# Kernel optimization log

Hardware: AMD Instinct MI355X
Metric: run time of the kernel (lower is better)

The kernel has to match this reference:

```python
import jax, jax.numpy as jnp
import numpy as np


def _pairwise_l2(x):
    # x: [N, D] -> [N, N] Euclidean distances, matching (x_i - x_j).norm(dim=-1)
    sq = jnp.sum(x * x, axis=-1)                      # [N]
    sqd = sq[:, None] + sq[None, :] - 2.0 * (x @ x.T)  # [N, N] squared distances
    sqd = jnp.maximum(sqd, 0.0)
    # safe sqrt: zero distance (diagonal) -> 0 with zero gradient, matching
    # torch's norm subgradient at 0
    pos = sqd > 0.0
    return jnp.where(pos, jnp.sqrt(jnp.where(pos, sqd, 1.0)), 0.0)


def setup_inputs() -> dict:
    key = jax.random.key(0)
    data = jax.random.normal(key, (8192, 256), dtype=jnp.float32)
    return {"data": data}


def reference(data) -> jnp.ndarray:
    x = data.reshape(data.shape[0], -1)               # [N, D]
    dist = _pairwise_l2(x)                            # [N, N]
    denom = jax.lax.stop_gradient(jnp.sum(dist, axis=1, keepdims=True))
    return dist / denom
```

## Files before the change

kernel.cpp:

```cpp
#include <hip/hip_runtime.h>
#include <stdint.h>

#define NN 8192
#define DD 256

typedef __attribute__((ext_vector_type(8))) short short8;
typedef __attribute__((ext_vector_type(4))) float f32x4;

typedef const uint32_t __attribute__((address_space(1)))* gbl_ptr_t;
typedef uint32_t __attribute__((address_space(3)))* lds_ptr_t;

__device__ __forceinline__ void gl_lds16(const void* g, const void* l) {
    __builtin_amdgcn_global_load_lds((gbl_ptr_t)(uintptr_t)g,
                                     (lds_ptr_t)(uintptr_t)l, 16, 0, 0);
}

__device__ __forceinline__ unsigned short f32_to_bf16(float f) {
    uint32_t u = __float_as_uint(f);
    u += 0x7fff + ((u >> 16) & 1);
    return (unsigned short)(u >> 16);
}
__device__ __forceinline__ float bf16_to_f32(unsigned short h) {
    return __uint_as_float(((uint32_t)h) << 16);
}

__global__ void prep_kernel(const float* __restrict__ x,
                            unsigned short* __restrict__ hi,
                            unsigned short* __restrict__ lo,
                            float* __restrict__ sq,
                            float* __restrict__ denom) {
    const int r = blockIdx.x;
    const int t = threadIdx.x;
    float v = x[(size_t)r * DD + t];
    unsigned short h = f32_to_bf16(v);
    unsigned short l = f32_to_bf16(v - bf16_to_f32(h));
    int csw = (t & ~63) | ((((t >> 3) & 7) ^ (r & 7)) << 3) | (t & 7);
    hi[(size_t)r * DD + csw] = h;
    lo[(size_t)r * DD + csw] = l;

    float s = v * v;
    #pragma unroll
    for (int m = 32; m >= 1; m >>= 1) s += __shfl_xor(s, m, 64);
    __shared__ float ws[4];
    if ((t & 63) == 0) ws[t >> 6] = s;
    __syncthreads();
    if (t == 0) {
        sq[r] = ws[0] + ws[1] + ws[2] + ws[3];
        denom[r] = 0.0f;
    }
}

__launch_bounds__(256, 2)
__global__ void dist_kernel(const unsigned short* __restrict__ hi,
                            const unsigned short* __restrict__ lo,
                            const float* __restrict__ sq,
                            float* __restrict__ out,
                            float* __restrict__ denom) {
    __shared__ __align__(16) unsigned short lds[4 * 128 * 64];
    unsigned short* ldsAhi = lds;
    unsigned short* ldsAlo = lds + 8192;
    unsigned short* ldsBhi = lds + 16384;
    unsigned short* ldsBlo = lds + 24576;

    const int tid  = threadIdx.x;
    const int lane = tid & 63;
    const int wid  = tid >> 6;
    const int wm = wid >> 1, wn = wid & 1;
    const int l15 = lane & 15, lk = lane >> 4;

    const int row0 = blockIdx.y * 128;
    const int col0 = blockIdx.x * 128;

    f32x4 acc[4][4];
    #pragma unroll
    for (int a = 0; a < 4; ++a)
        #pragma unroll
        for (int b = 0; b < 4; ++b) acc[a][b] = (f32x4){0.f, 0.f, 0.f, 0.f};

    float rsq[4][4], csq[4];
    #pragma unroll
    for (int fm = 0; fm < 4; ++fm)
        #pragma unroll
        for (int r = 0; r < 4; ++r)
            rsq[fm][r] = sq[row0 + wm * 64 + fm * 16 + lk * 4 + r];
    #pragma unroll
    for (int fn = 0; fn < 4; ++fn)
        csq[fn] = sq[col0 + wn * 64 + fn * 16 + l15];

    for (int kt = 0; kt < 4; ++kt) {
        #pragma unroll
        for (int c = 0; c < 4; ++c) {
            int lin  = c * 256 + tid;
            int row  = lin >> 3;
            int col8 = lin & 7;
            size_t goffA = (size_t)(row0 + row) * DD + kt * 64 + col8 * 8;
            size_t goffB = (size_t)(col0 + row) * DD + kt * 64 + col8 * 8;
            size_t lbyte = (size_t)(c * 256 + wid * 64) * 16;
            gl_lds16(hi + goffA, (const char*)ldsAhi + lbyte);
            gl_lds16(lo + goffA, (const char*)ldsAlo + lbyte);
            gl_lds16(hi + goffB, (const char*)ldsBhi + lbyte);
            gl_lds16(lo + goffB, (const char*)ldsBlo + lbyte);
        }
        __syncthreads();

        #pragma unroll
        for (int ks = 0; ks < 2; ++ks) {
            short8 ah[4], al[4], bh[4], bl[4];
            #pragma unroll
            for (int fm = 0; fm < 4; ++fm) {
                int row = wm * 64 + fm * 16 + l15;
                int cb  = (ks * 64 + lk * 16) ^ ((row & 7) << 4);
                int off = row * 64 + (cb >> 1);
                ah[fm] = *(const short8*)(ldsAhi + off);
                al[fm] = *(const short8*)(ldsAlo + off);
            }
            #pragma unroll
            for (int fn = 0; fn < 4; ++fn) {
                int row = wn * 64 + fn * 16 + l15;
                int cb  = (ks * 64 + lk * 16) ^ ((row & 7) << 4);
                int off = row * 64 + (cb >> 1);
                bh[fn] = *(const short8*)(ldsBhi + off);
                bl[fn] = *(const short8*)(ldsBlo + off);
            }
            #pragma unroll
            for (int fm = 0; fm < 4; ++fm)
                #pragma unroll
                for (int fn = 0; fn < 4; ++fn) {
                    acc[fm][fn] = __builtin_amdgcn_mfma_f32_16x16x32_bf16(
                        ah[fm], bh[fn], acc[fm][fn], 0, 0, 0);
                    acc[fm][fn] = __builtin_amdgcn_mfma_f32_16x16x32_bf16(
                        ah[fm], bl[fn], acc[fm][fn], 0, 0, 0);
                    acc[fm][fn] = __builtin_amdgcn_mfma_f32_16x16x32_bf16(
                        al[fm], bh[fn], acc[fm][fn], 0, 0, 0);
                }
        }
        __syncthreads();
    }

    float rp[4][4];
    #pragma unroll
    for (int a = 0; a < 4; ++a)
        #pragma unroll
        for (int b = 0; b < 4; ++b) rp[a][b] = 0.f;

    #pragma unroll
    for (int fm = 0; fm < 4; ++fm) {
        #pragma unroll
        for (int fn = 0; fn < 4; ++fn) {
            #pragma unroll
            for (int r = 0; r < 4; ++r) {
                float dot = acc[fm][fn][r];
                float sqd = rsq[fm][r] + csq[fn] - 2.0f * dot;
                sqd = fmaxf(sqd, 0.0f);
                float d = sqrtf(sqd);
                int grow = row0 + wm * 64 + fm * 16 + lk * 4 + r;
                int gcol = col0 + wn * 64 + fn * 16 + l15;
                out[(size_t)grow * NN + gcol] = d;
                rp[fm][r] += d;
            }
        }
    }
    #pragma unroll
    for (int fm = 0; fm < 4; ++fm)
        #pragma unroll
        for (int r = 0; r < 4; ++r) {
            float v = rp[fm][r];
            v += __shfl_xor(v, 1, 64);
            v += __shfl_xor(v, 2, 64);
            v += __shfl_xor(v, 4, 64);
            v += __shfl_xor(v, 8, 64);
            if (l15 == 0)
                atomicAdd(&denom[row0 + wm * 64 + fm * 16 + lk * 4 + r], v);
        }
}

__global__ void norm_kernel(float* __restrict__ out,
                            const float* __restrict__ denom) {
    const int total = NN * (NN / 4);
    float4* o4 = reinterpret_cast<float4*>(out);
    for (int i = blockIdx.x * blockDim.x + threadIdx.x; i < total;
         i += gridDim.x * blockDim.x) {
        int row = i >> 11;
        float inv = 1.0f / denom[row];
        float4 v = o4[i];
        v.x *= inv; v.y *= inv; v.z *= inv; v.w *= inv;
        o4[i] = v;
    }
}

extern "C" void kernel_launch(void* const* d_in, const int* in_sizes, int n_in,
                              void* d_out, int out_size, void* d_ws, size_t ws_size,
                              hipStream_t stream) {
    const float* x = (const float*)d_in[0];
    float* out = (float*)d_out;
    char* ws = (char*)d_ws;
    unsigned short* hi = (unsigned short*)ws;
    unsigned short* lo = (unsigned short*)(ws + (size_t)NN * DD * 2);
    float* sq    = (float*)(ws + (size_t)NN * DD * 4);
    float* denom = (float*)(ws + (size_t)NN * DD * 4 + NN * 4);

    prep_kernel<<<NN, 256, 0, stream>>>(x, hi, lo, sq, denom);
    dim3 g(NN / 128, NN / 128);
    dist_kernel<<<g, 256, 0, stream>>>(hi, lo, sq, out, denom);
    norm_kernel<<<2048, 256, 0, stream>>>(out, denom);
}
```

Before: 480.2 us.

## Exploit distance-matrix symmetry: compute upper-triangle tiles and write transposes

The distance kernel now launches only the upper-triangular set of 128x128 tiles (2080 instead of 4096). Each off-diagonal tile also accumulates column sums and writes its transposed copy through an XOR-swizzled LDS staging buffer. This roughly halves the triple-bf16 MFMA work, at the cost of a serial index-decode loop, extra LDS traffic and a second uncoalesced-free store pass. The normalisation is split into a small reciprocal kernel plus a fixed-stride, unrolled scaling kernel, so the per-element divide is dropped.

```diff
diff --git a/kernel.cpp b/kernel.cpp
--- a/kernel.cpp
+++ b/kernel.cpp
@@ -68,8 +68,12 @@
     const int wm = wid >> 1, wn = wid & 1;
     const int l15 = lane & 15, lk = lane >> 4;
 
-    const int row0 = blockIdx.y * 128;
-    const int col0 = blockIdx.x * 128;
+    int t = blockIdx.x, bi = 0;
+    while (t >= 64 - bi) { t -= 64 - bi; ++bi; }
+    const int bj = bi + t;
+    const int row0 = bi * 128;
+    const int col0 = bj * 128;
+    const bool offdiag = (bj > bi);
 
     f32x4 acc[4][4];
     #pragma unroll
@@ -137,11 +141,14 @@
         __syncthreads();
     }
 
-    float rp[4][4];
-    #pragma unroll
-    for (int a = 0; a < 4; ++a)
+    float rp[4][4], cp[4];
+    #pragma unroll
+    for (int a = 0; a < 4; ++a) {
+        cp[a] = 0.f;
         #pragma unroll
         for (int b = 0; b < 4; ++b) rp[a][b] = 0.f;
+    }
+    float* ldsT = reinterpret_cast<float*>(lds);
 
     #pragma unroll
     for (int fm = 0; fm < 4; ++fm) {
@@ -153,13 +160,18 @@
                 float sqd = rsq[fm][r] + csq[fn] - 2.0f * dot;
                 sqd = fmaxf(sqd, 0.0f);
                 float d = sqrtf(sqd);
-                int grow = row0 + wm * 64 + fm * 16 + lk * 4 + r;
-                int gcol = col0 + wn * 64 + fn * 16 + l15;
-                out[(size_t)grow * NN + gcol] = d;
+                int lr = wm * 64 + fm * 16 + lk * 4 + r;
+                int lc = wn * 64 + fn * 16 + l15;
+                out[(size_t)(row0 + lr) * NN + col0 + lc] = d;
                 rp[fm][r] += d;
+                if (offdiag) {
+                    cp[fn] += d;
+                    ldsT[lc * 128 + (lr ^ ((lc & 31) ^ ((lc & 4) << 2)))] = d;
+                }
             }
         }
     }
+
     #pragma unroll
     for (int fm = 0; fm < 4; ++fm)
         #pragma unroll
@@ -172,19 +184,44 @@
             if (l15 == 0)
                 atomicAdd(&denom[row0 + wm * 64 + fm * 16 + lk * 4 + r], v);
         }
+
+    if (offdiag) {
+        #pragma unroll
+        for (int fn = 0; fn < 4; ++fn) {
+            float v = cp[fn];
+            v += __shfl_xor(v, 16, 64);
+            v += __shfl_xor(v, 32, 64);
+            if (lane < 16)
+                atomicAdd(&denom[col0 + wn * 64 + fn * 16 + l15], v);
+        }
+        __syncthreads();
+        #pragma unroll
+        for (int it = 0; it < 64; ++it) {
+            int idx = it * 256 + tid;
+            int c  = idx >> 7;
+            int r_ = idx & 127;
+            float d = ldsT[c * 128 + (r_ ^ ((c & 31) ^ ((c & 4) << 2)))];
+            out[(size_t)(col0 + c) * NN + row0 + r_] = d;
+        }
+    }
+}
+
+__global__ void inv_kernel(float* __restrict__ denom) {
+    int i = blockIdx.x * 256 + threadIdx.x;
+    if (i < NN) denom[i] = 1.0f / denom[i];
 }
 
 __global__ void norm_kernel(float* __restrict__ out,
-                            const float* __restrict__ denom) {
-    const int total = NN * (NN / 4);
+                            const float* __restrict__ inv) {
+    const int i0 = blockIdx.x * blockDim.x + threadIdx.x;
     float4* o4 = reinterpret_cast<float4*>(out);
-    for (int i = blockIdx.x * blockDim.x + threadIdx.x; i < total;
-         i += gridDim.x * blockDim.x) {
-        int row = i >> 11;
-        float inv = 1.0f / denom[row];
-        float4 v = o4[i];
-        v.x *= inv; v.y *= inv; v.z *= inv; v.w *= inv;
-        o4[i] = v;
+    #pragma unroll
+    for (int k = 0; k < 8; ++k) {
+        int idx = k * 2097152 + i0;
+        float s = inv[idx >> 11];
+        float4 v = o4[idx];
+        v.x *= s; v.y *= s; v.z *= s; v.w *= s;
+        o4[idx] = v;
     }
 }
 
@@ -200,7 +237,7 @@
     float* denom = (float*)(ws + (size_t)NN * DD * 4 + NN * 4);
 
     prep_kernel<<<NN, 256, 0, stream>>>(x, hi, lo, sq, denom);
-    dim3 g(NN / 128, NN / 128);
-    dist_kernel<<<g, 256, 0, stream>>>(hi, lo, sq, out, denom);
-    norm_kernel<<<2048, 256, 0, stream>>>(out, denom);
-}
+    dist_kernel<<<2080, 256, 0, stream>>>(hi, lo, sq, out, denom);
+    inv_kernel<<<32, 256, 0, stream>>>(denom);
+    norm_kernel<<<8192, 256, 0, stream>>>(out, denom);
+}
```

Measured after the change: 426.6 us. -11.1%, faster.
